# Kernel optimization log

Hardware: AMD Instinct MI355X
Metric: run time of the kernel (lower is better)

Reference implementation:

```python
import jax, jax.numpy as jnp
import numpy as np

B, S, D = 8, 8192, 64
BUCKET = 64
N_HASHES = 8
N_BUCKETS = S // BUCKET  # 128, must be even
CAUSAL = True
NEG_LOOK = -1e38
NEG_SELF = -50000.0
EPS = 1e-6


def setup_inputs() -> dict:
    key = jax.random.key(0)
    k1, k2, k3 = jax.random.split(key, 3)
    qk = jax.random.normal(k1, (B, S, D), jnp.float32)
    v = jax.random.normal(k2, (B, S, D), jnp.float32)
    # random rotations for LSH hashing: (dim, n_hashes, n_buckets//2)
    rotations = jax.random.normal(k3, (D, N_HASHES, N_BUCKETS // 2), jnp.float32)
    return {"qk": qk, "v": v, "rotations": rotations}


def _look_one_back(x):
    # concat each chunk with the previous chunk (wrap-around), along axis 2
    x_extra = jnp.roll(x, 1, axis=1)
    return jnp.concatenate([x, x_extra], axis=2)


def reference(qk, v, rotations):
    batch, seqlen, dim = qk.shape
    n_bins = N_BUCKETS
    chunks = N_HASHES * n_bins

    # ---- hash_vectors ----
    rotated = jnp.einsum('btf,fhi->bhti', qk, rotations)          # [B,H,S,nb/2]
    rotated = jnp.concatenate([rotated, -rotated], axis=-1)       # [B,H,S,nb]
    buckets = jnp.argmax(rotated, axis=-1)                        # [B,H,S]
    offsets = (jnp.arange(N_HASHES) * N_BUCKETS)[None, :, None]
    buckets = (buckets + offsets).reshape(batch, -1)              # [B,H*S]

    # ---- sort by (bucket, position) ----
    ticker = jnp.arange(N_HASHES * seqlen)
    buckets_and_t = seqlen * buckets + (ticker % seqlen)[None, :]
    sticker = jnp.argsort(buckets_and_t, axis=-1, stable=True)    # [B,H*S]
    undo_sort = jnp.argsort(sticker, axis=-1, stable=True)
    st = sticker % seqlen                                         # original positions

    sqk = jnp.take_along_axis(qk, st[..., None], axis=1)          # [B,H*S,D]
    sv = jnp.take_along_axis(v, st[..., None], axis=1)

    bq_t = st.reshape(batch, chunks, -1)                          # [B,C,bucket]
    bqk = sqk.reshape(batch, chunks, -1, dim)
    bv = sv.reshape(batch, chunks, -1, dim)

    bq = bqk
    bk = bqk * jax.lax.rsqrt(jnp.sum(bqk * bqk, axis=-1, keepdims=True) + EPS)

    bk = _look_one_back(bk)                                       # [B,C,2*bucket,D]
    bv = _look_one_back(bv)
    bkv_t = _look_one_back(bq_t[..., None])[..., 0]               # [B,C,2*bucket]

    dots = jnp.einsum('bhie,bhje->bhij', bq, bk) * (dim ** -0.5)  # [B,C,bucket,2*bucket]
    if CAUSAL:
        causal_mask = bq_t[:, :, :, None] < bkv_t[:, :, None, :]
        dots = jnp.where(causal_mask, NEG_LOOK, dots)
    self_mask = bq_t[:, :, :, None] == bkv_t[:, :, None, :]
    dots = jnp.where(self_mask, NEG_SELF, dots)

    dots_lse = jax.nn.logsumexp(dots, axis=-1, keepdims=True)
    probs = jnp.exp(dots - dots_lse)
    bo = jnp.einsum('buij,buje->buie', probs, bv)                 # [B,C,bucket,D]

    so = bo.reshape(batch, -1, dim)                               # [B,H*S,D]
    slogits = dots_lse.reshape(batch, -1)                         # [B,H*S]

    # ---- unsort ----
    o = jnp.take_along_axis(so, undo_sort[..., None], axis=1)
    logits = jnp.take_along_axis(slogits, undo_sort, axis=1)

    # ---- combine hash rounds via logsumexp weights ----
    o = o.reshape(batch, N_HASHES, seqlen, dim)
    logits = logits.reshape(batch, N_HASHES, seqlen, 1)
    w = jnp.exp(logits - jax.nn.logsumexp(logits, axis=1, keepdims=True))
    out = jnp.sum(o * w, axis=1)                                  # [B,S,D]
    return out
```

## Files before the change

### kernel.cpp

```cpp
#include <hip/hip_runtime.h>
#include <cstdint>
#include <cstddef>

#define BB 8
#define SS 8192
#define DD 64
#define HH 8
#define NB 128
#define NCHUNK 128
#define CHUNKS 1024

typedef __attribute__((ext_vector_type(8))) short bf16x8;
typedef __attribute__((ext_vector_type(4))) float f32x4;

__device__ __forceinline__ unsigned short f2b(float x) {
  union { float f; unsigned int u; } c; c.f = x;
  unsigned int r = c.u + 0x7fffu + ((c.u >> 16) & 1u);
  return (unsigned short)(r >> 16);
}
__device__ __forceinline__ float b2f(unsigned short h) {
  union { unsigned int u; float f; } c; c.u = ((unsigned int)h) << 16;
  return c.f;
}

__global__ __launch_bounds__(256) void prep_kernel(const float* __restrict__ qk,
                                                   const float* __restrict__ v,
                                                   unsigned short* __restrict__ qhat,
                                                   unsigned short* __restrict__ vb,
                                                   float* __restrict__ snorm) {
  const int idx = blockIdx.x * 256 + threadIdx.x;
  const int row = idx >> 3, seg = idx & 7;
  const size_t base = (size_t)row * DD + seg * 8;

  float4 a0 = ((const float4*)(qk + base))[0];
  float4 a1 = ((const float4*)(qk + base))[1];
  float vals[8] = {a0.x, a0.y, a0.z, a0.w, a1.x, a1.y, a1.z, a1.w};
  float ssq = 0.f;
#pragma unroll
  for (int k = 0; k < 8; ++k) ssq += vals[k] * vals[k];
  ssq += __shfl_xor(ssq, 1);
  ssq += __shfl_xor(ssq, 2);
  ssq += __shfl_xor(ssq, 4);
  const float r = rsqrtf(ssq + 1e-6f);
  const float sn = (ssq + 1e-6f) * r;
  uint4 qo;
  unsigned int* qp = (unsigned int*)&qo;
#pragma unroll
  for (int k = 0; k < 4; ++k)
    qp[k] = (unsigned int)f2b(vals[2 * k] * r) | ((unsigned int)f2b(vals[2 * k + 1] * r) << 16);
  *(uint4*)(qhat + base) = qo;
  if (seg == 0) snorm[row] = sn;

  float4 v0 = ((const float4*)(v + base))[0];
  float4 v1 = ((const float4*)(v + base))[1];
  float vv[8] = {v0.x, v0.y, v0.z, v0.w, v1.x, v1.y, v1.z, v1.w};
  uint4 vo;
  unsigned int* vp = (unsigned int*)&vo;
#pragma unroll
  for (int k = 0; k < 4; ++k)
    vp[k] = (unsigned int)f2b(vv[2 * k]) | ((unsigned int)f2b(vv[2 * k + 1]) << 16);
  *(uint4*)(vb + base) = vo;
}

__global__ __launch_bounds__(256) void rott_kernel(const float* __restrict__ rot,
                                                   float* __restrict__ rotT) {
  __shared__ float tile[64][68];
  const int tid = threadIdx.x;
  const int hi0 = blockIdx.x * 64;
#pragma unroll
  for (int rep = 0; rep < 4; ++rep) {
    const int j = rep * 256 + tid;
    const int f = j >> 4, c4 = (j & 15) * 4;
    const float4 vv = *(const float4*)(rot + (size_t)f * (HH * 64) + hi0 + c4);
    *(float4*)&tile[f][c4] = vv;
  }
  __syncthreads();
#pragma unroll
  for (int rep = 0; rep < 4; ++rep) {
    const int j = rep * 256 + tid;
    const int c = j >> 4, f4 = (j & 15) * 4;
    float4 o;
    o.x = tile[f4 + 0][c];
    o.y = tile[f4 + 1][c];
    o.z = tile[f4 + 2][c];
    o.w = tile[f4 + 3][c];
    *(float4*)(rotT + (size_t)(hi0 + c) * 64 + f4) = o;
  }
}

#define TH 0.03125f
__global__ __launch_bounds__(256, 4) void hash_kernel(const float* __restrict__ qk,
                                                      const float* __restrict__ rotT,
                                                      unsigned char* __restrict__ bucket) {
  __shared__ __align__(16) unsigned short qh[64][72];
  __shared__ __align__(16) unsigned short ql[64][72];
  __shared__ __align__(16) unsigned short rh[64][72];
  __shared__ __align__(16) unsigned short rl[64][72];
  const int tid = threadIdx.x;
  const int b = blockIdx.y, tile = blockIdx.x;

  {
    const int row = tid >> 2, fs = (tid & 3) * 16;
    const float* src = qk + ((size_t)b * SS + (size_t)tile * 64 + row) * DD + fs;
    unsigned short hi16[16], lo16[16];
#pragma unroll
    for (int k = 0; k < 4; ++k) {
      float4 v = ((const float4*)src)[k];
      const float xs[4] = {v.x, v.y, v.z, v.w};
#pragma unroll
      for (int e = 0; e < 4; ++e) {
        const float x = xs[e];
        const unsigned short hb = f2b(x);
        hi16[k * 4 + e] = hb;
        lo16[k * 4 + e] = f2b(x - b2f(hb));
      }
    }
    *(uint4*)&qh[row][fs] = *(uint4*)&hi16[0];
    *(uint4*)&qh[row][fs + 8] = *(uint4*)&hi16[8];
    *(uint4*)&ql[row][fs] = *(uint4*)&lo16[0];
    *(uint4*)&ql[row][fs + 8] = *(uint4*)&lo16[8];
  }

  const int lane = tid & 63, w = tid >> 6;
  const int r16 = lane & 15, g = lane >> 4;

  for (int h = 0; h < HH; ++h) {
    __syncthreads();
    {
      const int c = tid >> 2, fs = (tid & 3) * 16;
      const float* src = rotT + (size_t)(h * 64 + c) * DD + fs;
      unsigned short hi16[16], lo16[16];
#pragma unroll
      for (int k = 0; k < 4; ++k) {
        float4 v = ((const float4*)src)[k];
        const float xs[4] = {v.x, v.y, v.z, v.w};
#pragma unroll
        for (int e = 0; e < 4; ++e) {
          const float x = xs[e];
          const unsigned short hb = f2b(x);
          hi16[k * 4 + e] = hb;
          lo16[k * 4 + e] = f2b(x - b2f(hb));
        }
      }
      *(uint4*)&rh[c][fs] = *(uint4*)&hi16[0];
      *(uint4*)&rh[c][fs + 8] = *(uint4*)&hi16[8];
      *(uint4*)&rl[c][fs] = *(uint4*)&lo16[0];
      *(uint4*)&rl[c][fs + 8] = *(uint4*)&lo16[8];
    }
    __syncthreads();

    bf16x8 qh0 = *(const bf16x8*)&qh[16 * w + r16][g * 8];
    bf16x8 qh1 = *(const bf16x8*)&qh[16 * w + r16][32 + g * 8];
    bf16x8 ql0 = *(const bf16x8*)&ql[16 * w + r16][g * 8];
    bf16x8 ql1 = *(const bf16x8*)&ql[16 * w + r16][32 + g * 8];

    f32x4 acc[4];
#pragma unroll
    for (int n = 0; n < 4; ++n) acc[n] = (f32x4){0.f, 0.f, 0.f, 0.f};
#pragma unroll
    for (int n = 0; n < 4; ++n) {
      bf16x8 rh0 = *(const bf16x8*)&rh[16 * n + r16][g * 8];
      bf16x8 rh1 = *(const bf16x8*)&rh[16 * n + r16][32 + g * 8];
      bf16x8 rl0 = *(const bf16x8*)&rl[16 * n + r16][g * 8];
      bf16x8 rl1 = *(const bf16x8*)&rl[16 * n + r16][32 + g * 8];
      acc[n] = __builtin_amdgcn_mfma_f32_16x16x32_bf16(qh0, rh0, acc[n], 0, 0, 0);
      acc[n] = __builtin_amdgcn_mfma_f32_16x16x32_bf16(qh0, rl0, acc[n], 0, 0, 0);
      acc[n] = __builtin_amdgcn_mfma_f32_16x16x32_bf16(ql0, rh0, acc[n], 0, 0, 0);
      acc[n] = __builtin_amdgcn_mfma_f32_16x16x32_bf16(qh1, rh1, acc[n], 0, 0, 0);
      acc[n] = __builtin_amdgcn_mfma_f32_16x16x32_bf16(qh1, rl1, acc[n], 0, 0, 0);
      acc[n] = __builtin_amdgcn_mfma_f32_16x16x32_bf16(ql1, rh1, acc[n], 0, 0, 0);
    }

#pragma unroll
    for (int i = 0; i < 4; ++i) {
      const int row = 16 * w + 4 * g + i;
      float bv = -3.4e38f;
      int bi = 0;
#pragma unroll
      for (int n = 0; n < 4; ++n) {
        const float vp = acc[n][i];
        const int ip = 16 * n + r16;
        if (vp > bv || (vp == bv && ip < bi)) { bv = vp; bi = ip; }
      }
#pragma unroll
      for (int n = 0; n < 4; ++n) {
        const float vn = -acc[n][i];
        const int in_ = 16 * n + r16 + 64;
        if (vn > bv || (vn == bv && in_ < bi)) { bv = vn; bi = in_; }
      }
#pragma unroll
      for (int off = 1; off < 16; off <<= 1) {
        const float ov = __shfl_xor(bv, off);
        const int oi = __shfl_xor(bi, off);
        if (ov > bv || (ov == bv && oi < bi)) { bv = ov; bi = oi; }
      }
      bool other = false;
#pragma unroll
      for (int n = 0; n < 4; ++n) {
        other |= (acc[n][i] >= bv - TH) && (16 * n + r16 != bi);
        other |= (-acc[n][i] >= bv - TH) && (16 * n + r16 + 64 != bi);
      }
      const unsigned long long bal = __ballot(other);
      const bool need = ((bal >> (16 * g)) & 0xFFFFull) != 0ull;
      if (need) {
        const int trow = tile * 64 + row;
        const float* qrow = qk + ((size_t)b * SS + trow) * DD;
        float mv = -3.4e38f;
        int mi = 9999;
#pragma unroll
        for (int n = 0; n < 4; ++n) {
          const bool cp = (acc[n][i] >= bv - TH);
          const bool cn = (-acc[n][i] >= bv - TH);
          if (cp || cn) {
            const int c = 16 * n + r16;
            const float* rrow = rotT + (size_t)(h * 64 + c) * DD;
            float d = 0.f;
#pragma unroll 1
            for (int f4 = 0; f4 < 16; ++f4) {
              const float4 qv = *(const float4*)(qrow + 4 * f4);
              const float4 rv = *(const float4*)(rrow + 4 * f4);
              d = fmaf(qv.x, rv.x, d);
              d = fmaf(qv.y, rv.y, d);
              d = fmaf(qv.z, rv.z, d);
              d = fmaf(qv.w, rv.w, d);
            }
            if (cp && (d > mv || (d == mv && c < mi))) { mv = d; mi = c; }
            const float dn = -d;
            if (cn && (dn > mv || (dn == mv && (c + 64) < mi))) { mv = dn; mi = c + 64; }
          }
        }
#pragma unroll
        for (int off = 1; off < 16; off <<= 1) {
          const float ov = __shfl_xor(mv, off);
          const int oi = __shfl_xor(mi, off);
          if (ov > mv || (ov == mv && oi < mi)) { mv = ov; mi = oi; }
        }
        bi = mi;
      }
      if (r16 == 0)
        bucket[((size_t)(b * HH + h)) * SS + (size_t)tile * 64 + row] = (unsigned char)bi;
    }
  }
}

__global__ __launch_bounds__(1024) void sort_kernel(const unsigned char* __restrict__ bucket,
                                                    int* __restrict__ sticker) {
  __shared__ unsigned char lb[SS];
  __shared__ unsigned int hist[NB * NCHUNK];
  __shared__ unsigned int ssum[1024];
  const int tid = threadIdx.x;
  const int bh = blockIdx.x;

  if (tid < 512)
    ((uint4*)lb)[tid] = ((const uint4*)(bucket + (size_t)bh * SS))[tid];
#pragma unroll
  for (int k = 0; k < (NB * NCHUNK) / 1024; ++k) hist[tid + k * 1024] = 0u;
  __syncthreads();

#pragma unroll
  for (int rep = 0; rep < SS / 1024; ++rep) {
    const int t = rep * 1024 + tid;
    atomicAdd(&hist[(int)lb[t] * NCHUNK + (t >> 6)], 1u);
  }
  __syncthreads();

  unsigned int segsum = 0u;
  const int base = tid * 16;
#pragma unroll
  for (int e = 0; e < 16; ++e) segsum += hist[base + e];
  ssum[tid] = segsum;
  __syncthreads();
  for (int off = 1; off < 1024; off <<= 1) {
    const unsigned int vv = (tid >= off) ? ssum[tid - off] : 0u;
    __syncthreads();
    ssum[tid] += vv;
    __syncthreads();
  }
  unsigned int run = ssum[tid] - segsum;
#pragma unroll
  for (int e = 0; e < 16; ++e) {
    const unsigned int tv = hist[base + e];
    hist[base + e] = run;
    run += tv;
  }
  __syncthreads();

  const int wid = tid >> 6, lane = tid & 63;
#pragma unroll
  for (int rep = 0; rep < NCHUNK / 16; ++rep) {
    const int c = rep * 16 + wid;
    const int t = c * 64 + lane;
    const int bk = lb[t];
    unsigned long long mm = ~0ull;
#pragma unroll
    for (int bit = 0; bit < 7; ++bit) {
      const unsigned long long bal = __ballot((bk >> bit) & 1);
      mm &= ((bk >> bit) & 1) ? bal : ~bal;
    }
    const int rank = __popcll(mm & ((1ull << lane) - 1ull));
    const int pos = (int)hist[bk * NCHUNK + c] + rank;
    sticker[(size_t)bh * SS + pos] = t;
  }
}

__global__ __launch_bounds__(256) void attn_kernel(const unsigned short* __restrict__ qhat,
                                                   const unsigned short* __restrict__ vb,
                                                   const float* __restrict__ snorm,
                                                   const int* __restrict__ sticker,
                                                   unsigned short* __restrict__ so,
                                                   float* __restrict__ slogits,
                                                   const int b_base) {
  __shared__ __align__(16) unsigned short kbps[128 * 72];
  __shared__ __align__(16) unsigned short vt[64][136];
  __shared__ int st[128];
  __shared__ float sn_s[64];
  const int tid = threadIdx.x;
  const int bin = blockIdx.y, bl = blockIdx.x, h = blockIdx.z;
  const int b = b_base + bl;
  const int bh = b * HH + h;
  const int prev = (h * NB + bin + CHUNKS - 1) & (CHUNKS - 1);
  const int ph = prev >> 7, pbin = prev & 127;

  if (tid < 128) {
    const int j = tid;
    const int src = (j < 64) ? (bh * SS + bin * 64 + j)
                             : ((b * HH + ph) * SS + pbin * 64 + (j - 64));
    st[j] = sticker[src];
  }
  __syncthreads();

  {
    const int row = tid >> 1, half = tid & 1;
    const int trow = st[row];
    {
      const uint4* qsrc = (const uint4*)(qhat + ((size_t)b * SS + trow) * DD) + half * 4;
      uint4 q0 = qsrc[0], q1 = qsrc[1], q2 = qsrc[2], q3 = qsrc[3];
      unsigned short* kd = &kbps[row * 72 + half * 32];
      *(uint4*)&kd[0] = q0;
      *(uint4*)&kd[8] = q1;
      *(uint4*)&kd[16] = q2;
      *(uint4*)&kd[24] = q3;
    }
    {
      const uint4* vsrc = (const uint4*)(vb + ((size_t)b * SS + trow) * DD) + half * 4;
      uint4 w0 = vsrc[0], w1 = vsrc[1], w2 = vsrc[2], w3 = vsrc[3];
      unsigned int uu[16] = {w0.x, w0.y, w0.z, w0.w, w1.x, w1.y, w1.z, w1.w,
                             w2.x, w2.y, w2.z, w2.w, w3.x, w3.y, w3.z, w3.w};
#pragma unroll
      for (int m = 0; m < 16; ++m) {
        vt[half * 32 + 2 * m][row] = (unsigned short)(uu[m] & 0xffffu);
        vt[half * 32 + 2 * m + 1][row] = (unsigned short)(uu[m] >> 16);
      }
    }
  }
  if (tid < 64) sn_s[tid] = snorm[(size_t)b * SS + st[tid]];
  __syncthreads();

  const int lane = tid & 63, w = tid >> 6;
  const int r16 = lane & 15, g = lane >> 4;

  f32x4 acc[8];
#pragma unroll
  for (int n = 0; n < 8; ++n) acc[n] = (f32x4){0.f, 0.f, 0.f, 0.f};
  bf16x8 af0 = *(const bf16x8*)&kbps[(16 * w + r16) * 72 + g * 8];
  bf16x8 af1 = *(const bf16x8*)&kbps[(16 * w + r16) * 72 + 32 + g * 8];
#pragma unroll
  for (int n = 0; n < 8; ++n) {
    bf16x8 bf0 = *(const bf16x8*)&kbps[(16 * n + r16) * 72 + g * 8];
    bf16x8 bf1 = *(const bf16x8*)&kbps[(16 * n + r16) * 72 + 32 + g * 8];
    acc[n] = __builtin_amdgcn_mfma_f32_16x16x32_bf16(af0, bf0, acc[n], 0, 0, 0);
    acc[n] = __builtin_amdgcn_mfma_f32_16x16x32_bf16(af1, bf1, acc[n], 0, 0, 0);
  }

  int tkj[8];
#pragma unroll
  for (int n = 0; n < 8; ++n) tkj[n] = st[16 * n + r16];

  float lse4[4];
#pragma unroll
  for (int i = 0; i < 4; ++i) {
    const int q = 16 * w + 4 * g + i;
    const int tq = st[q];
    const float sq = sn_s[q] * 0.125f;
    float mm = -3.4e38f;
#pragma unroll
    for (int n = 0; n < 8; ++n) {
      float s = acc[n][i] * sq;
      s = (tkj[n] > tq) ? -1e38f : ((tkj[n] == tq) ? -50000.f : s);
      acc[n][i] = s;
      mm = fmaxf(mm, s);
    }
    mm = fmaxf(mm, __shfl_xor(mm, 1));
    mm = fmaxf(mm, __shfl_xor(mm, 2));
    mm = fmaxf(mm, __shfl_xor(mm, 4));
    mm = fmaxf(mm, __shfl_xor(mm, 8));
    float sum = 0.f;
#pragma unroll
    for (int n = 0; n < 8; ++n) sum += __expf(acc[n][i] - mm);
    sum += __shfl_xor(sum, 1);
    sum += __shfl_xor(sum, 2);
    sum += __shfl_xor(sum, 4);
    sum += __shfl_xor(sum, 8);
    const float lse = mm + logf(sum);
    lse4[i] = lse;
#pragma unroll
    for (int n = 0; n < 8; ++n) acc[n][i] = __expf(acc[n][i] - lse);
  }

  __syncthreads();

#pragma unroll
  for (int i = 0; i < 4; ++i) {
    const int q = 16 * w + 4 * g + i;
#pragma unroll
    for (int n = 0; n < 8; ++n)
      kbps[q * 136 + 16 * n + r16] = f2b(acc[n][i]);
  }
  if (r16 == 0) {
#pragma unroll
    for (int i = 0; i < 4; ++i) {
      const int q = 16 * w + 4 * g + i;
      slogits[((size_t)b * SS + st[q]) * HH + h] = lse4[i];
    }
  }
  __syncthreads();

  f32x4 o[4];
#pragma unroll
  for (int n = 0; n < 4; ++n) o[n] = (f32x4){0.f, 0.f, 0.f, 0.f};
#pragma unroll
  for (int kk = 0; kk < 4; ++kk) {
    bf16x8 pa = *(const bf16x8*)&kbps[(16 * w + r16) * 136 + kk * 32 + g * 8];
#pragma unroll
    for (int n = 0; n < 4; ++n) {
      bf16x8 vbf = *(const bf16x8*)&vt[16 * n + r16][kk * 32 + g * 8];
      o[n] = __builtin_amdgcn_mfma_f32_16x16x32_bf16(pa, vbf, o[n], 0, 0, 0);
    }
  }

  __syncthreads();
#pragma unroll
  for (int i = 0; i < 4; ++i) {
    const int q = 16 * w + 4 * g + i;
#pragma unroll
    for (int n = 0; n < 4; ++n)
      kbps[q * 72 + 16 * n + r16] = f2b(o[n][i]);
  }
  __syncthreads();

  {
    const int row = tid >> 2, q4 = tid & 3;
    uint4 x0 = *(const uint4*)&kbps[row * 72 + q4 * 16];
    uint4 x1 = *(const uint4*)&kbps[row * 72 + q4 * 16 + 8];
    unsigned short* dst = so + (((size_t)bl * SS + st[row]) * HH + h) * DD + q4 * 16;
    *(uint4*)&dst[0] = x0;
    *(uint4*)&dst[8] = x1;
  }
}

__global__ __launch_bounds__(256) void gather_out_kernel(const unsigned short* __restrict__ so,
                                                         const float* __restrict__ slogits,
                                                         float* __restrict__ out,
                                                         const int b_base) {
  const int idx = blockIdx.x * 256 + threadIdx.x;
  const int seg = idx & 7;
  const int btl = idx >> 3;

  const float* lrow = slogits + ((size_t)b_base * SS + btl) * HH;
  float4 l0 = ((const float4*)lrow)[0];
  float4 l1 = ((const float4*)lrow)[1];
  float l[8] = {l0.x, l0.y, l0.z, l0.w, l1.x, l1.y, l1.z, l1.w};
  float m = -3.4e38f;
#pragma unroll
  for (int h = 0; h < HH; ++h) m = fmaxf(m, l[h]);
  float sum = 0.f;
#pragma unroll
  for (int h = 0; h < HH; ++h) sum += __expf(l[h] - m);
  const float lse = m + logf(sum);

  float acc[8];
#pragma unroll
  for (int k = 0; k < 8; ++k) acc[k] = 0.f;
#pragma unroll
  for (int h = 0; h < HH; ++h) {
    const float wgt = __expf(l[h] - lse);
    uint4 u = *(const uint4*)(so + ((size_t)btl * HH + h) * DD + seg * 8);
    const unsigned int uu[4] = {u.x, u.y, u.z, u.w};
#pragma unroll
    for (int k = 0; k < 4; ++k) {
      acc[2 * k] += wgt * b2f((unsigned short)(uu[k] & 0xffffu));
      acc[2 * k + 1] += wgt * b2f((unsigned short)(uu[k] >> 16));
    }
  }
  float* dst = out + ((size_t)b_base * SS + btl) * DD + seg * 8;
  float4 o0, o1;
  o0.x = acc[0]; o0.y = acc[1]; o0.z = acc[2]; o0.w = acc[3];
  o1.x = acc[4]; o1.y = acc[5]; o1.z = acc[6]; o1.w = acc[7];
  ((float4*)dst)[0] = o0;
  ((float4*)dst)[1] = o1;
}

extern "C" void kernel_launch(void* const* d_in, const int* in_sizes, int n_in,
                              void* d_out, int out_size, void* d_ws, size_t ws_size,
                              hipStream_t stream) {
  (void)in_sizes; (void)n_in; (void)out_size; (void)ws_size;
  const float* qk = (const float*)d_in[0];
  const float* v = (const float*)d_in[1];
  const float* rot = (const float*)d_in[2];
  float* out = (float*)d_out;

  char* ws = (char*)d_ws;
  int* sticker = (int*)ws;
  float* slogits = (float*)(ws + ((size_t)2 << 20));
  float* snorm = (float*)(ws + ((size_t)4 << 20));
  unsigned char* bucket = (unsigned char*)(ws + ((size_t)4 << 20) + ((size_t)256 << 10));
  float* rotT = (float*)(ws + ((size_t)4 << 20) + ((size_t)768 << 10));
  unsigned short* qhat = (unsigned short*)(ws + ((size_t)5 << 20));
  unsigned short* vb = (unsigned short*)(ws + ((size_t)13 << 20));
  unsigned short* so = (unsigned short*)(ws + ((size_t)21 << 20));

  rott_kernel<<<8, 256, 0, stream>>>(rot, rotT);
  prep_kernel<<<(BB * SS * 8) / 256, 256, 0, stream>>>(qk, v, qhat, vb, snorm);
  hash_kernel<<<dim3(NCHUNK, BB), 256, 0, stream>>>(qk, rotT, bucket);
  sort_kernel<<<BB * HH, 1024, 0, stream>>>(bucket, sticker);

  for (int half = 0; half < 2; ++half) {
    const int b_base = half * (BB / 2);
    attn_kernel<<<dim3(BB / 2, NB, HH), 256, 0, stream>>>(qhat, vb, snorm, sticker, so, slogits, b_base);
    gather_out_kernel<<<(BB / 2 * SS * 8) / 256, 256, 0, stream>>>(so, slogits, out, b_base);
  }
}
```

Measured before the change: 186.2 us.

## Precompute bf16 hi/lo splits upstream and drop LDS staging in hash kernel

Moves the bf16 hi/lo split of qk into prep_kernel and of the rotations into rott_kernel, writing them to new workspace buffers. hash_kernel now loads MFMA fragments straight from global memory and no longer uses shared memory or __syncthreads per hash round. The argmax is also reworked as an abs-max reduction followed by a min-index pass plus a candidate count. The exact fp32 fallback now fires whenever two or more candidates fall inside the threshold, rather than only when a candidate other than the winner does. The trade-off is extra global writes and reads of 16 MB for the q splits, and uncached global loads for the rotation fragments that every block re-reads.

```diff
diff --git a/kernel.cpp b/kernel.cpp
--- a/kernel.cpp
+++ b/kernel.cpp
@@ -27,6 +27,8 @@
                                                    const float* __restrict__ v,
                                                    unsigned short* __restrict__ qhat,
                                                    unsigned short* __restrict__ vb,
+                                                   unsigned short* __restrict__ qhi,
+                                                   unsigned short* __restrict__ qlo,
                                                    float* __restrict__ snorm) {
   const int idx = blockIdx.x * 256 + threadIdx.x;
   const int row = idx >> 3, seg = idx & 7;
@@ -51,6 +53,21 @@
   *(uint4*)(qhat + base) = qo;
   if (seg == 0) snorm[row] = sn;
 
+  uint4 ho, lo4;
+  unsigned int* hp = (unsigned int*)&ho;
+  unsigned int* lp = (unsigned int*)&lo4;
+#pragma unroll
+  for (int k = 0; k < 4; ++k) {
+    const unsigned short h0 = f2b(vals[2 * k]);
+    const unsigned short h1 = f2b(vals[2 * k + 1]);
+    const unsigned short l0 = f2b(vals[2 * k] - b2f(h0));
+    const unsigned short l1 = f2b(vals[2 * k + 1] - b2f(h1));
+    hp[k] = (unsigned int)h0 | ((unsigned int)h1 << 16);
+    lp[k] = (unsigned int)l0 | ((unsigned int)l1 << 16);
+  }
+  *(uint4*)(qhi + base) = ho;
+  *(uint4*)(qlo + base) = lo4;
+
   float4 v0 = ((const float4*)(v + base))[0];
   float4 v1 = ((const float4*)(v + base))[1];
   float vv[8] = {v0.x, v0.y, v0.z, v0.w, v1.x, v1.y, v1.z, v1.w};
@@ -63,7 +80,9 @@
 }
 
 __global__ __launch_bounds__(256) void rott_kernel(const float* __restrict__ rot,
-                                                   float* __restrict__ rotT) {
+                                                   float* __restrict__ rotT,
+                                                   unsigned short* __restrict__ rhiT,
+                                                   unsigned short* __restrict__ rloT) {
   __shared__ float tile[64][68];
   const int tid = threadIdx.x;
   const int hi0 = blockIdx.x * 64;
@@ -85,84 +104,55 @@
     o.z = tile[f4 + 2][c];
     o.w = tile[f4 + 3][c];
     *(float4*)(rotT + (size_t)(hi0 + c) * 64 + f4) = o;
+    const float xs[4] = {o.x, o.y, o.z, o.w};
+    unsigned int hpack[2], lpack[2];
+#pragma unroll
+    for (int e = 0; e < 2; ++e) {
+      const unsigned short h0 = f2b(xs[2 * e]);
+      const unsigned short h1 = f2b(xs[2 * e + 1]);
+      const unsigned short l0 = f2b(xs[2 * e] - b2f(h0));
+      const unsigned short l1 = f2b(xs[2 * e + 1] - b2f(h1));
+      hpack[e] = (unsigned int)h0 | ((unsigned int)h1 << 16);
+      lpack[e] = (unsigned int)l0 | ((unsigned int)l1 << 16);
+    }
+    uint2 hv; hv.x = hpack[0]; hv.y = hpack[1];
+    uint2 lv; lv.x = lpack[0]; lv.y = lpack[1];
+    *(uint2*)&rhiT[(size_t)(hi0 + c) * 64 + f4] = hv;
+    *(uint2*)&rloT[(size_t)(hi0 + c) * 64 + f4] = lv;
   }
 }
 
 #define TH 0.03125f
-__global__ __launch_bounds__(256, 4) void hash_kernel(const float* __restrict__ qk,
-                                                      const float* __restrict__ rotT,
-                                                      unsigned char* __restrict__ bucket) {
-  __shared__ __align__(16) unsigned short qh[64][72];
-  __shared__ __align__(16) unsigned short ql[64][72];
-  __shared__ __align__(16) unsigned short rh[64][72];
-  __shared__ __align__(16) unsigned short rl[64][72];
+__global__ __launch_bounds__(256) void hash_kernel(const float* __restrict__ qk,
+                                                   const float* __restrict__ rotT,
+                                                   const unsigned short* __restrict__ qhi,
+                                                   const unsigned short* __restrict__ qlo,
+                                                   const unsigned short* __restrict__ rhiT,
+                                                   const unsigned short* __restrict__ rloT,
+                                                   unsigned char* __restrict__ bucket) {
   const int tid = threadIdx.x;
   const int b = blockIdx.y, tile = blockIdx.x;
-
-  {
-    const int row = tid >> 2, fs = (tid & 3) * 16;
-    const float* src = qk + ((size_t)b * SS + (size_t)tile * 64 + row) * DD + fs;
-    unsigned short hi16[16], lo16[16];
-#pragma unroll
-    for (int k = 0; k < 4; ++k) {
-      float4 v = ((const float4*)src)[k];
-      const float xs[4] = {v.x, v.y, v.z, v.w};
-#pragma unroll
-      for (int e = 0; e < 4; ++e) {
-        const float x = xs[e];
-        const unsigned short hb = f2b(x);
-        hi16[k * 4 + e] = hb;
-        lo16[k * 4 + e] = f2b(x - b2f(hb));
-      }
-    }
-    *(uint4*)&qh[row][fs] = *(uint4*)&hi16[0];
-    *(uint4*)&qh[row][fs + 8] = *(uint4*)&hi16[8];
-    *(uint4*)&ql[row][fs] = *(uint4*)&lo16[0];
-    *(uint4*)&ql[row][fs + 8] = *(uint4*)&lo16[8];
-  }
-
+  const int tile64 = tile * 64;
   const int lane = tid & 63, w = tid >> 6;
   const int r16 = lane & 15, g = lane >> 4;
 
+  const size_t qoff = ((size_t)b * SS + tile64 + 16 * w + r16) * DD;
+  const bf16x8 qh0 = *(const bf16x8*)(qhi + qoff + g * 8);
+  const bf16x8 qh1 = *(const bf16x8*)(qhi + qoff + 32 + g * 8);
+  const bf16x8 ql0 = *(const bf16x8*)(qlo + qoff + g * 8);
+  const bf16x8 ql1 = *(const bf16x8*)(qlo + qoff + 32 + g * 8);
+
   for (int h = 0; h < HH; ++h) {
-    __syncthreads();
-    {
-      const int c = tid >> 2, fs = (tid & 3) * 16;
-      const float* src = rotT + (size_t)(h * 64 + c) * DD + fs;
-      unsigned short hi16[16], lo16[16];
-#pragma unroll
-      for (int k = 0; k < 4; ++k) {
-        float4 v = ((const float4*)src)[k];
-        const float xs[4] = {v.x, v.y, v.z, v.w};
-#pragma unroll
-        for (int e = 0; e < 4; ++e) {
-          const float x = xs[e];
-          const unsigned short hb = f2b(x);
-          hi16[k * 4 + e] = hb;
-          lo16[k * 4 + e] = f2b(x - b2f(hb));
-        }
-      }
-      *(uint4*)&rh[c][fs] = *(uint4*)&hi16[0];
-      *(uint4*)&rh[c][fs + 8] = *(uint4*)&hi16[8];
-      *(uint4*)&rl[c][fs] = *(uint4*)&lo16[0];
-      *(uint4*)&rl[c][fs + 8] = *(uint4*)&lo16[8];
-    }
-    __syncthreads();
-
-    bf16x8 qh0 = *(const bf16x8*)&qh[16 * w + r16][g * 8];
-    bf16x8 qh1 = *(const bf16x8*)&qh[16 * w + r16][32 + g * 8];
-    bf16x8 ql0 = *(const bf16x8*)&ql[16 * w + r16][g * 8];
-    bf16x8 ql1 = *(const bf16x8*)&ql[16 * w + r16][32 + g * 8];
-
     f32x4 acc[4];
 #pragma unroll
     for (int n = 0; n < 4; ++n) acc[n] = (f32x4){0.f, 0.f, 0.f, 0.f};
 #pragma unroll
     for (int n = 0; n < 4; ++n) {
-      bf16x8 rh0 = *(const bf16x8*)&rh[16 * n + r16][g * 8];
-      bf16x8 rh1 = *(const bf16x8*)&rh[16 * n + r16][32 + g * 8];
-      bf16x8 rl0 = *(const bf16x8*)&rl[16 * n + r16][g * 8];
-      bf16x8 rl1 = *(const bf16x8*)&rl[16 * n + r16][32 + g * 8];
+      const size_t roff = (size_t)(h * 64 + 16 * n + r16) * DD;
+      const bf16x8 rh0 = *(const bf16x8*)(rhiT + roff + g * 8);
+      const bf16x8 rh1 = *(const bf16x8*)(rhiT + roff + 32 + g * 8);
+      const bf16x8 rl0 = *(const bf16x8*)(rloT + roff + g * 8);
+      const bf16x8 rl1 = *(const bf16x8*)(rloT + roff + 32 + g * 8);
       acc[n] = __builtin_amdgcn_mfma_f32_16x16x32_bf16(qh0, rh0, acc[n], 0, 0, 0);
       acc[n] = __builtin_amdgcn_mfma_f32_16x16x32_bf16(qh0, rl0, acc[n], 0, 0, 0);
       acc[n] = __builtin_amdgcn_mfma_f32_16x16x32_bf16(ql0, rh0, acc[n], 0, 0, 0);
@@ -174,39 +164,41 @@
 #pragma unroll
     for (int i = 0; i < 4; ++i) {
       const int row = 16 * w + 4 * g + i;
-      float bv = -3.4e38f;
-      int bi = 0;
+      float bv = fmaxf(fmaxf(fabsf(acc[0][i]), fabsf(acc[1][i])),
+                       fmaxf(fabsf(acc[2][i]), fabsf(acc[3][i])));
+#pragma unroll
+      for (int off = 1; off < 16; off <<= 1)
+        bv = fmaxf(bv, __shfl_xor(bv, off));
+
+      int mi = 9999;
 #pragma unroll
       for (int n = 0; n < 4; ++n) {
-        const float vp = acc[n][i];
-        const int ip = 16 * n + r16;
-        if (vp > bv || (vp == bv && ip < bi)) { bv = vp; bi = ip; }
+        const float vv = acc[n][i];
+        const int c = 16 * n + r16;
+        const int idx = (vv < 0.f) ? (c + 64) : c;
+        if (fabsf(vv) == bv && idx < mi) mi = idx;
       }
 #pragma unroll
+      for (int off = 1; off < 16; off <<= 1) {
+        const int om = __shfl_xor(mi, off);
+        mi = (om < mi) ? om : mi;
+      }
+
+      int cnt = 0;
+#pragma unroll
       for (int n = 0; n < 4; ++n) {
-        const float vn = -acc[n][i];
-        const int in_ = 16 * n + r16 + 64;
-        if (vn > bv || (vn == bv && in_ < bi)) { bv = vn; bi = in_; }
+        cnt += (acc[n][i] >= bv - TH) ? 1 : 0;
+        cnt += (-acc[n][i] >= bv - TH) ? 1 : 0;
       }
 #pragma unroll
-      for (int off = 1; off < 16; off <<= 1) {
-        const float ov = __shfl_xor(bv, off);
-        const int oi = __shfl_xor(bi, off);
-        if (ov > bv || (ov == bv && oi < bi)) { bv = ov; bi = oi; }
-      }
-      bool other = false;
-#pragma unroll
-      for (int n = 0; n < 4; ++n) {
-        other |= (acc[n][i] >= bv - TH) && (16 * n + r16 != bi);
-        other |= (-acc[n][i] >= bv - TH) && (16 * n + r16 + 64 != bi);
-      }
-      const unsigned long long bal = __ballot(other);
-      const bool need = ((bal >> (16 * g)) & 0xFFFFull) != 0ull;
-      if (need) {
-        const int trow = tile * 64 + row;
-        const float* qrow = qk + ((size_t)b * SS + trow) * DD;
+      for (int off = 1; off < 16; off <<= 1)
+        cnt += __shfl_xor(cnt, off);
+
+      int bi = mi;
+      if (cnt >= 2) {
+        const float* qrow = qk + ((size_t)b * SS + tile64 + row) * DD;
         float mv = -3.4e38f;
-        int mi = 9999;
+        int fmi = 9999;
 #pragma unroll
         for (int n = 0; n < 4; ++n) {
           const bool cp = (acc[n][i] >= bv - TH);
@@ -224,21 +216,21 @@
               d = fmaf(qv.z, rv.z, d);
               d = fmaf(qv.w, rv.w, d);
             }
-            if (cp && (d > mv || (d == mv && c < mi))) { mv = d; mi = c; }
+            if (cp && (d > mv || (d == mv && c < fmi))) { mv = d; fmi = c; }
             const float dn = -d;
-            if (cn && (dn > mv || (dn == mv && (c + 64) < mi))) { mv = dn; mi = c + 64; }
+            if (cn && (dn > mv || (dn == mv && (c + 64) < fmi))) { mv = dn; fmi = c + 64; }
           }
         }
 #pragma unroll
         for (int off = 1; off < 16; off <<= 1) {
           const float ov = __shfl_xor(mv, off);
-          const int oi = __shfl_xor(mi, off);
-          if (ov > mv || (ov == mv && oi < mi)) { mv = ov; mi = oi; }
+          const int oi = __shfl_xor(fmi, off);
+          if (ov > mv || (ov == mv && oi < fmi)) { mv = ov; fmi = oi; }
         }
-        bi = mi;
+        bi = fmi;
       }
       if (r16 == 0)
-        bucket[((size_t)(b * HH + h)) * SS + (size_t)tile * 64 + row] = (unsigned char)bi;
+        bucket[((size_t)(b * HH + h)) * SS + tile64 + row] = (unsigned char)bi;
     }
   }
 }
@@ -515,13 +507,17 @@
   float* snorm = (float*)(ws + ((size_t)4 << 20));
   unsigned char* bucket = (unsigned char*)(ws + ((size_t)4 << 20) + ((size_t)256 << 10));
   float* rotT = (float*)(ws + ((size_t)4 << 20) + ((size_t)768 << 10));
+  unsigned short* rhiT = (unsigned short*)(ws + ((size_t)4 << 20) + ((size_t)896 << 10));
+  unsigned short* rloT = (unsigned short*)(ws + ((size_t)4 << 20) + ((size_t)960 << 10));
   unsigned short* qhat = (unsigned short*)(ws + ((size_t)5 << 20));
   unsigned short* vb = (unsigned short*)(ws + ((size_t)13 << 20));
-  unsigned short* so = (unsigned short*)(ws + ((size_t)21 << 20));
-
-  rott_kernel<<<8, 256, 0, stream>>>(rot, rotT);
-  prep_kernel<<<(BB * SS * 8) / 256, 256, 0, stream>>>(qk, v, qhat, vb, snorm);
-  hash_kernel<<<dim3(NCHUNK, BB), 256, 0, stream>>>(qk, rotT, bucket);
+  unsigned short* qhi = (unsigned short*)(ws + ((size_t)21 << 20));
+  unsigned short* qlo = (unsigned short*)(ws + ((size_t)29 << 20));
+  unsigned short* so = (unsigned short*)(ws + ((size_t)37 << 20));
+
+  rott_kernel<<<8, 256, 0, stream>>>(rot, rotT, rhiT, rloT);
+  prep_kernel<<<(BB * SS * 8) / 256, 256, 0, stream>>>(qk, v, qhat, vb, qhi, qlo, snorm);
+  hash_kernel<<<dim3(NCHUNK, BB), 256, 0, stream>>>(qk, rotT, qhi, qlo, rhiT, rloT, bucket);
   sort_kernel<<<BB * HH, 1024, 0, stream>>>(bucket, sticker);
 
   for (int half = 0; half < 2; ++half) {
```

Result: slower. 208.0 us (+11.7%).
